# Optimization experiments

Hardware: AMD Instinct MI355X
Metric: run time of the kernel (lower is better)

## Reference

```python
import jax, jax.numpy as jnp
import numpy as np

B = 8192
NOISE = 25


def setup_inputs() -> dict:
    key = jax.random.key(0)
    ks = jax.random.split(key, 16)
    rn = lambda k, s: jax.random.normal(k, s, dtype=jnp.float32)
    return {
        "z": rn(ks[0], (B, 3)),
        "z_next": rn(ks[1], (B, 3)),
        "n": rn(ks[2], (B, NOISE)),
        "prior": rn(ks[3], (B, 4611)),
        "w1_W": rn(ks[4], (NOISE, 192)) * 0.2, "w1_b": rn(ks[5], (192,)) * 0.1,
        "b1_W": rn(ks[6], (NOISE, 64)) * 0.2, "b1_b": rn(ks[7], (64,)) * 0.1,
        "w2_W": rn(ks[8], (NOISE, 4096)) * 0.2, "w2_b": rn(ks[9], (4096,)) * 0.1,
        "b2_W": rn(ks[10], (NOISE, 64)) * 0.2, "b2_b": rn(ks[11], (64,)) * 0.1,
        "w3_W": rn(ks[12], (NOISE, 192)) * 0.2, "w3_b": rn(ks[13], (192,)) * 0.1,
        "b3_W": rn(ks[14], (NOISE, 3)) * 0.2, "b3_b": rn(ks[15], (3,)) * 0.1,
    }


def _pairwise_dist(A, Bm):
    # sqrt(sum_d (A_i - B_j)^2 + 1e-8) computed via the norm identity -> one GEMM
    sq = (jnp.sum(A * A, axis=1)[:, None]
          + jnp.sum(Bm * Bm, axis=1)[None, :]
          - 2.0 * (A @ Bm.T))
    return jnp.sqrt(jnp.maximum(sq, 0.0) + 1e-8)


def reference(z, z_next, n, prior,
              w1_W, w1_b, b1_W, b1_b,
              w2_W, w2_b, b2_W, b2_b,
              w3_W, w3_b, b3_W, b3_b):
    bs = z.shape[0]
    # hypernetwork: per-sample decoder weights from noise n (B, 25)
    W1 = (n @ w1_W + w1_b).reshape(bs, 64, 3)
    B1 = n @ b1_W + b1_b                       # (B, 64)
    W2 = (n @ w2_W + w2_b).reshape(bs, 64, 64)
    B2 = n @ b2_W + b2_b                       # (B, 64)
    W3 = (n @ w3_W + w3_b).reshape(bs, 3, 64)
    B3 = n @ b3_W + b3_b                       # (B, 3)
    # decode: per-sample bmm chain with ELU
    h = jax.nn.elu(jnp.einsum('bij,bj->bi', W1, z) + B1)
    h = jax.nn.elu(jnp.einsum('bij,bj->bi', W2, h) + B2)
    z_hat = jnp.einsum('bij,bj->bi', W3, h) + B3
    recon = jnp.mean(jnp.sum((z_hat - z_next) ** 2, axis=1))
    # KL estimator over flattened generated weights, D = 4611
    G = jnp.concatenate([W1.reshape(bs, -1), B1, W2.reshape(bs, -1), B2,
                         W3.reshape(bs, -1), B3], axis=1)
    wp = jnp.min(_pairwise_dist(prior, G), axis=0)   # nearest prior sample per gen sample
    idx = jnp.arange(bs)
    ww_mat = _pairwise_dist(G, G).at[idx, idx].add(1e10)
    ww = jnp.min(ww_mat, axis=0)
    D = G.shape[1]
    kl = jnp.mean(jnp.log(wp / (ww + 1e-8) + 1e-8)) * D
    kl = kl + jnp.log(jnp.float32(bs) / jnp.float32(bs - 1))
    return recon, kl, z_hat
```

## Files before the change

### kernel.cpp

```cpp
#include <hip/hip_runtime.h>
#include <math.h>

#define BATCH 8192
#define D_G   4611
#define DGP   4624
#define KN    25
#define KE    28

#define WS_WCAT   0
#define WS_BCAT   115600
#define WS_WCATT  120224
#define WS_M      249344
#define WS_C      249984
#define WS_BB     250016
#define WS_PPAD   250048
#define WS_Q      479424
#define WS_G2     487616
#define WS_RPAD   495808
#define WS_WP2    725184
#define WS_WW2    733376
#define WS_ACC    741568
#define WS_H1T    741600
#define WS_H2T    1265888

__device__ inline float eluf(float x) { return x > 0.f ? x : expm1f(x); }

__device__ __forceinline__ void gload_lds16(const float* g, float* l) {
  __builtin_amdgcn_global_load_lds((const __attribute__((address_space(1))) unsigned int*)g,
                                   (__attribute__((address_space(3))) unsigned int*)l, 16, 0, 0);
}

__device__ inline float sdot26(const float* __restrict__ WT, int rowidx, const float* nx) {
  const float* row = WT + (size_t)__builtin_amdgcn_readfirstlane(rowidx) * KE;
  float acc = row[25];
#pragma unroll
  for (int k = 0; k < 25; k++) acc = fmaf(row[k], nx[k], acc);
  return acc;
}

__global__ void k_init(float* ws) {
  int idx = blockIdx.x * 256 + threadIdx.x;
  unsigned int* u = (unsigned int*)ws;
  if (idx < BATCH)            u[WS_WP2 + idx] = 0x7F7FFFFFu;
  else if (idx < 2 * BATCH)   u[WS_WW2 + (idx - BATCH)] = 0x7F7FFFFFu;
  else if (idx == 2 * BATCH)  ws[WS_ACC] = 0.f;
}

__global__ void k_build(const float* __restrict__ w1W, const float* __restrict__ w1b,
                        const float* __restrict__ b1W, const float* __restrict__ b1b,
                        const float* __restrict__ w2W, const float* __restrict__ w2b,
                        const float* __restrict__ b2W, const float* __restrict__ b2b,
                        const float* __restrict__ w3W, const float* __restrict__ w3b,
                        const float* __restrict__ b3W, const float* __restrict__ b3b,
                        float* ws) {
  int idx = blockIdx.x * 256 + threadIdx.x;
  if (idx >= KN * D_G) return;
  int k = idx / D_G;
  int d = idx - k * D_G;
  float wv, bv;
  if (d < 192)       { int c = d;        wv = w1W[k*192  + c]; bv = w1b[c]; }
  else if (d < 256)  { int c = d - 192;  wv = b1W[k*64   + c]; bv = b1b[c]; }
  else if (d < 4352) { int c = d - 256;  wv = w2W[k*4096 + c]; bv = w2b[c]; }
  else if (d < 4416) { int c = d - 4352; wv = b2W[k*64   + c]; bv = b2b[c]; }
  else if (d < 4608) { int c = d - 4416; wv = w3W[k*192  + c]; bv = w3b[c]; }
  else               { int c = d - 4608; wv = b3W[k*3    + c]; bv = b3b[c]; }
  ws[WS_WCAT  + k * DGP + d] = wv;
  ws[WS_WCATT + d * KE  + k] = wv;
  if (k == 0) {
    ws[WS_BCAT + d] = bv;
    ws[WS_WCATT + d * KE + 25] = bv;
    ws[WS_WCATT + d * KE + 26] = 0.f;
    ws[WS_WCATT + d * KE + 27] = 0.f;
  }
}

__global__ __launch_bounds__(256) void k_M(float* ws) {
  const float* Wc = ws + WS_WCAT;
  const float* bc = ws + WS_BCAT;
  __shared__ float part[4][26];
  int a = blockIdx.x, t = threadIdx.x;
  int wv = t >> 6, l = t & 63;
  if (a < 25) {
    float acc[26];
#pragma unroll
    for (int v = 0; v < 26; v++) acc[v] = 0.f;
    for (int d = t; d < D_G; d += 256) {
      float va = Wc[a * DGP + d];
#pragma unroll
      for (int b = 0; b < 25; b++) acc[b] += va * Wc[b * DGP + d];
      acc[25] += va * bc[d];
    }
#pragma unroll
    for (int v = 0; v < 26; v++) {
      float x = acc[v];
#pragma unroll
      for (int off = 32; off > 0; off >>= 1) x += __shfl_down(x, off, 64);
      if (l == 0) part[wv][v] = x;
    }
    __syncthreads();
    if (t < 26) {
      float s = part[0][t] + part[1][t] + part[2][t] + part[3][t];
      if (t < 25) ws[WS_M + a * 25 + t] = s; else ws[WS_C + a] = s;
    }
  } else {
    float acc = 0.f;
    for (int d = t; d < D_G; d += 256) { float b = bc[d]; acc += b * b; }
#pragma unroll
    for (int off = 32; off > 0; off >>= 1) acc += __shfl_down(acc, off, 64);
    if (l == 0) part[wv][0] = acc;
    __syncthreads();
    if (t == 0) ws[WS_BB] = part[0][0] + part[1][0] + part[2][0] + part[3][0];
  }
}

__global__ void k_persample(const float* __restrict__ n, float* ws) {
  int j = blockIdx.x * 256 + threadIdx.x;
  if (j >= BATCH) return;
  const float* M  = ws + WS_M;
  const float* cv = ws + WS_C;
  float nr[25];
#pragma unroll
  for (int k = 0; k < 25; k++) nr[k] = n[j * 25 + k];
  float q = 0.f;
  for (int k2 = 0; k2 < 25; k2++) {
    float p = 0.f;
#pragma unroll
    for (int k1 = 0; k1 < 25; k1++) p += nr[k1] * M[k1 * 25 + k2];
    ws[WS_PPAD + j * KE + k2] = p;
    q += p * nr[k2];
  }
  float nc = 0.f;
#pragma unroll
  for (int k = 0; k < 25; k++) nc += nr[k] * cv[k];
  ws[WS_PPAD + j * KE + 25] = -0.5f * q;
  ws[WS_PPAD + j * KE + 26] = 0.f;
  ws[WS_PPAD + j * KE + 27] = 0.f;
  ws[WS_Q  + j] = q;
  ws[WS_G2 + j] = q + 2.f * nc + ws[WS_BB];
}

__global__ __launch_bounds__(256, 2) void k_prior(const float* __restrict__ prior, float* ws) {
  __shared__ float wlds[2][26 * 256 + 512];
  const float* wc = ws + WS_WCAT;
  const float* bc = ws + WS_BCAT;
  int t = threadIdx.x;
  int wv = t >> 6, l = t & 63;
  int i0 = (blockIdx.x * 4 + wv) * 4;
  const float* pr0 = prior + (size_t)i0 * D_G;

  float racc[4][25];
  float sacc[4], p2acc[4];
#pragma unroll
  for (int r = 0; r < 4; r++) {
    sacc[r] = 0.f; p2acc[r] = 0.f;
#pragma unroll
    for (int k = 0; k < 25; k++) racc[r][k] = 0.f;
  }

  float pvC[4][4], pvN[4][4];

#pragma unroll
  for (int u = 0; u < 7; u++) {
    int row = u * 4 + wv;
    if (row < 26)
      gload_lds16(wc + (size_t)row * DGP + 4 * l, &wlds[0][row * 256]);
  }
#pragma unroll
  for (int r = 0; r < 4; r++)
#pragma unroll
    for (int q = 0; q < 4; q++)
      pvN[r][q] = pr0[(size_t)r * D_G + 4 * l + q];

  for (int ch = 0; ch < 18; ++ch) {
    int cur = ch & 1;
    __syncthreads();
#pragma unroll
    for (int r = 0; r < 4; r++)
#pragma unroll
      for (int q = 0; q < 4; q++) pvC[r][q] = pvN[r][q];
    if (ch < 17) {
      int dnext = (ch + 1) * 256;
#pragma unroll
      for (int u = 0; u < 7; u++) {
        int row = u * 4 + wv;
        if (row < 26)
          gload_lds16(wc + (size_t)row * DGP + dnext + 4 * l, &wlds[cur ^ 1][row * 256]);
      }
#pragma unroll
      for (int r = 0; r < 4; r++)
#pragma unroll
        for (int q = 0; q < 4; q++)
          pvN[r][q] = pr0[(size_t)r * D_G + dnext + 4 * l + q];
    }
    const float* wb = wlds[cur];
    float4 bl = *(const float4*)&wb[25 * 256 + 4 * l];
#pragma unroll
    for (int r = 0; r < 4; r++) {
      p2acc[r] += pvC[r][0]*pvC[r][0] + pvC[r][1]*pvC[r][1] + pvC[r][2]*pvC[r][2] + pvC[r][3]*pvC[r][3];
      sacc[r]  += pvC[r][0]*bl.x + pvC[r][1]*bl.y + pvC[r][2]*bl.z + pvC[r][3]*bl.w;
    }
#pragma unroll
    for (int k = 0; k < 25; k++) {
      float4 w = *(const float4*)&wb[k * 256 + 4 * l];
#pragma unroll
      for (int r = 0; r < 4; r++)
        racc[r][k] += pvC[r][0]*w.x + pvC[r][1]*w.y + pvC[r][2]*w.z + pvC[r][3]*w.w;
    }
  }
  if (l < 3) {
    int d = 4608 + l;
#pragma unroll
    for (int r = 0; r < 4; r++) {
      float pvt = pr0[(size_t)r * D_G + d];
      p2acc[r] += pvt * pvt;
      sacc[r]  += pvt * bc[d];
#pragma unroll
      for (int k = 0; k < 25; k++) racc[r][k] += pvt * wc[(size_t)k * DGP + d];
    }
  }
#pragma unroll
  for (int r = 0; r < 4; r++) {
#pragma unroll
    for (int k = 0; k < 25; k++) {
      float v = racc[r][k];
#pragma unroll
      for (int off = 32; off > 0; off >>= 1) v += __shfl_down(v, off, 64);
      if (l == 0) ws[WS_RPAD + (size_t)(i0 + r) * KE + k] = v;
    }
    float s = sacc[r], p2 = p2acc[r];
#pragma unroll
    for (int off = 32; off > 0; off >>= 1) { s += __shfl_down(s, off, 64); p2 += __shfl_down(p2, off, 64); }
    if (l == 0) {
      ws[WS_RPAD + (size_t)(i0 + r) * KE + 25] = -0.5f * (p2 - 2.f * s);
      ws[WS_RPAD + (size_t)(i0 + r) * KE + 26] = 0.f;
      ws[WS_RPAD + (size_t)(i0 + r) * KE + 27] = 0.f;
    }
  }
}

template <int SKIP>
__global__ __launch_bounds__(256) void k_pair(const float* __restrict__ APAD,
                                              const float* __restrict__ Bn,
                                              const float* __restrict__ beta,
                                              unsigned int* __restrict__ outm) {
  __shared__ float rows[256 * KE] __attribute__((aligned(16)));
  int t = threadIdx.x;
  int jbase = blockIdx.y * 256;
  {
    const float4* src = (const float4*)(APAD + (size_t)jbase * KE);
    float4* dst = (float4*)rows;
#pragma unroll
    for (int u = 0; u < 7; u++) dst[t + 256 * u] = src[t + 256 * u];
  }
  int j0 = blockIdx.x * 512 + t;
  int j1 = j0 + 256;
  float nx0[25], nx1[25];
#pragma unroll
  for (int k = 0; k < 25; k++) { nx0[k] = Bn[j0 * 25 + k]; nx1[k] = Bn[j1 * 25 + k]; }
  float bj0 = beta[j0], bj1 = beta[j1];
  float mn0 = 3.402823466e38f, mn1 = 3.402823466e38f;
  __syncthreads();
#pragma unroll 2
  for (int it = 0; it < 256; ++it) {
    const float4* rv = (const float4*)(rows + it * KE);
    float rw[28];
#pragma unroll
    for (int u = 0; u < 7; u++) *(float4*)&rw[4 * u] = rv[u];
    float a0 = rw[25], a1 = rw[25];
#pragma unroll
    for (int k = 0; k < 25; k++) { a0 = fmaf(rw[k], nx0[k], a0); a1 = fmaf(rw[k], nx1[k], a1); }
    float sq0 = fmaxf(fmaf(-2.f, a0, bj0), 0.f);
    float sq1 = fmaxf(fmaf(-2.f, a1, bj1), 0.f);
    int i = jbase + it;
    bool sk0 = SKIP && (i == j0);
    bool sk1 = SKIP && (i == j1);
    mn0 = sk0 ? mn0 : fminf(mn0, sq0);
    mn1 = sk1 ? mn1 : fminf(mn1, sq1);
  }
  atomicMin(&outm[j0], __float_as_uint(mn0));
  atomicMin(&outm[j1], __float_as_uint(mn1));
}

__global__ __launch_bounds__(64) void kd1(const float* __restrict__ n, const float* __restrict__ z,
                                          const float* __restrict__ ws_wt, float* __restrict__ h1t) {
  int s = blockIdx.x * 64 + threadIdx.x;
  int rb = blockIdx.y * 16;
  float nx[25];
#pragma unroll
  for (int k = 0; k < 25; k++) nx[k] = n[s * 25 + k];
  float zr[3];
#pragma unroll
  for (int d = 0; d < 3; d++) zr[d] = z[s * 3 + d];
  for (int r = 0; r < 16; r++) {
    int rr = rb + r;
    float acc = sdot26(ws_wt, 192 + rr, nx);
#pragma unroll
    for (int d = 0; d < 3; d++)
      acc = fmaf(sdot26(ws_wt, rr * 3 + d, nx), zr[d], acc);
    h1t[rr * BATCH + s] = eluf(acc);
  }
}

__global__ __launch_bounds__(64) void kd2(const float* __restrict__ n,
                                          const float* __restrict__ ws_wt,
                                          const float* __restrict__ h1t, float* __restrict__ h2t) {
  int s = blockIdx.x * 64 + threadIdx.x;
  int rb = blockIdx.y * 4;
  float nx[25];
#pragma unroll
  for (int k = 0; k < 25; k++) nx[k] = n[s * 25 + k];
  float acc[4];
#pragma unroll
  for (int r = 0; r < 4; r++) acc[r] = sdot26(ws_wt, 4352 + rb + r, nx);
  for (int c = 0; c < 64; c++) {
    float h1c = h1t[c * BATCH + s];
#pragma unroll
    for (int r = 0; r < 4; r++) {
      float w = sdot26(ws_wt, 256 + (rb + r) * 64 + c, nx);
      acc[r] = fmaf(w, h1c, acc[r]);
    }
  }
#pragma unroll
  for (int r = 0; r < 4; r++) h2t[(rb + r) * BATCH + s] = eluf(acc[r]);
}

__global__ __launch_bounds__(64) void kd3(const float* __restrict__ n,
                                          const float* __restrict__ znext,
                                          const float* __restrict__ ws_wt,
                                          const float* __restrict__ h2t,
                                          float* __restrict__ out, float* __restrict__ accum) {
  int s = blockIdx.x * 64 + threadIdx.x;
  int r = blockIdx.y;
  float nx[25];
#pragma unroll
  for (int k = 0; k < 25; k++) nx[k] = n[s * 25 + k];
  float acc = sdot26(ws_wt, 4608 + r, nx);
  for (int c = 0; c < 64; c++)
    acc = fmaf(sdot26(ws_wt, 4416 + r * 64 + c, nx), h2t[c * BATCH + s], acc);
  out[2 + s * 3 + r] = acc;
  float dz = acc - znext[s * 3 + r];
  float v = dz * dz;
#pragma unroll
  for (int off = 32; off > 0; off >>= 1) v += __shfl_down(v, off, 64);
  if (threadIdx.x == 0) atomicAdd(accum, v);
}

__global__ void k_finish(float* ws, float* __restrict__ out) {
  __shared__ float sred[256];
  int t = threadIdx.x;
  float part = 0.f;
  for (int j = t; j < BATCH; j += 256) {
    float wp2 = ws[WS_WP2 + j];
    float ww2 = ws[WS_WW2 + j];
    float wp = sqrtf(wp2 + 1e-8f);
    float ww = sqrtf(ww2 + 1e-8f);
    part += logf(wp / (ww + 1e-8f) + 1e-8f);
  }
  sred[t] = part; __syncthreads();
  for (int off = 128; off > 0; off >>= 1) { if (t < off) sred[t] += sred[t + off]; __syncthreads(); }
  if (t == 0) {
    float kl = sred[0] / (float)BATCH * (float)D_G + logf((float)BATCH / (float)(BATCH - 1));
    out[0] = ws[WS_ACC] / (float)BATCH;
    out[1] = kl;
  }
}

extern "C" void kernel_launch(void* const* d_in, const int* in_sizes, int n_in,
                              void* d_out, int out_size, void* d_ws, size_t ws_size,
                              hipStream_t stream) {
  (void)in_sizes; (void)n_in; (void)out_size; (void)ws_size;
  const float* z     = (const float*)d_in[0];
  const float* znext = (const float*)d_in[1];
  const float* n     = (const float*)d_in[2];
  const float* prior = (const float*)d_in[3];
  const float* w1W = (const float*)d_in[4];  const float* w1b = (const float*)d_in[5];
  const float* b1W = (const float*)d_in[6];  const float* b1b = (const float*)d_in[7];
  const float* w2W = (const float*)d_in[8];  const float* w2b = (const float*)d_in[9];
  const float* b2W = (const float*)d_in[10]; const float* b2b = (const float*)d_in[11];
  const float* w3W = (const float*)d_in[12]; const float* w3b = (const float*)d_in[13];
  const float* b3W = (const float*)d_in[14]; const float* b3b = (const float*)d_in[15];
  float* out = (float*)d_out;
  float* ws  = (float*)d_ws;

  k_init<<<dim3(65), dim3(256), 0, stream>>>(ws);
  k_build<<<dim3((KN * D_G + 255) / 256), dim3(256), 0, stream>>>(
      w1W, w1b, b1W, b1b, w2W, w2b, b2W, b2b, w3W, w3b, b3W, b3b, ws);
  k_M<<<dim3(26), dim3(256), 0, stream>>>(ws);
  k_persample<<<dim3(32), dim3(256), 0, stream>>>(n, ws);
  k_prior<<<dim3(512), dim3(256), 0, stream>>>(prior, ws);
  k_pair<1><<<dim3(16, 32), dim3(256), 0, stream>>>(ws + WS_PPAD, n, ws + WS_Q,
                                                    (unsigned int*)(ws + WS_WW2));
  k_pair<0><<<dim3(16, 32), dim3(256), 0, stream>>>(ws + WS_RPAD, n, ws + WS_G2,
                                                    (unsigned int*)(ws + WS_WP2));
  kd1<<<dim3(128, 4), dim3(64), 0, stream>>>(n, z, ws + WS_WCATT, ws + WS_H1T);
  kd2<<<dim3(128, 16), dim3(64), 0, stream>>>(n, ws + WS_WCATT, ws + WS_H1T, ws + WS_H2T);
  kd3<<<dim3(128, 3), dim3(64), 0, stream>>>(n, znext, ws + WS_WCATT, ws + WS_H2T, out, ws + WS_ACC);
  k_finish<<<dim3(1), dim3(256), 0, stream>>>(ws, out);
}
```

Baseline: 546.4 us.

## Retile pairwise min kernel to 4 columns per thread with transposed noise

The pairwise-distance min kernel now gives each thread 4 columns instead of 2 and uses 128-row tiles instead of 256. This halves the LDS row tile and raises register reuse of each loaded row. Noise is stored transposed (k-major) in k_persample so the per-thread noise loads coalesce. The init kernel is folded into k_build to save a launch. The NT buffer aliases the H1T region, which is safe only because kd1 writes H1T after k_pair runs. Register pressure rises to about 100 noise values per thread, which could reduce occupancy.

```diff
diff --git a/kernel.cpp b/kernel.cpp
--- a/kernel.cpp
+++ b/kernel.cpp
@@ -21,6 +21,7 @@
 #define WS_WW2    733376
 #define WS_ACC    741568
 #define WS_H1T    741600
+#define WS_NT     741600
 #define WS_H2T    1265888
 
 __device__ inline float eluf(float x) { return x > 0.f ? x : expm1f(x); }
@@ -36,14 +37,6 @@
 #pragma unroll
   for (int k = 0; k < 25; k++) acc = fmaf(row[k], nx[k], acc);
   return acc;
-}
-
-__global__ void k_init(float* ws) {
-  int idx = blockIdx.x * 256 + threadIdx.x;
-  unsigned int* u = (unsigned int*)ws;
-  if (idx < BATCH)            u[WS_WP2 + idx] = 0x7F7FFFFFu;
-  else if (idx < 2 * BATCH)   u[WS_WW2 + (idx - BATCH)] = 0x7F7FFFFFu;
-  else if (idx == 2 * BATCH)  ws[WS_ACC] = 0.f;
 }
 
 __global__ void k_build(const float* __restrict__ w1W, const float* __restrict__ w1b,
@@ -54,6 +47,10 @@
                         const float* __restrict__ b3W, const float* __restrict__ b3b,
                         float* ws) {
   int idx = blockIdx.x * 256 + threadIdx.x;
+  unsigned int* u = (unsigned int*)ws;
+  if (idx < BATCH)            u[WS_WP2 + idx] = 0x7F7FFFFFu;
+  else if (idx < 2 * BATCH)   u[WS_WW2 + (idx - BATCH)] = 0x7F7FFFFFu;
+  else if (idx == 2 * BATCH)  ws[WS_ACC] = 0.f;
   if (idx >= KN * D_G) return;
   int k = idx / D_G;
   int d = idx - k * D_G;
@@ -121,6 +118,8 @@
   float nr[25];
 #pragma unroll
   for (int k = 0; k < 25; k++) nr[k] = n[j * 25 + k];
+#pragma unroll
+  for (int k = 0; k < 25; k++) ws[WS_NT + k * BATCH + j] = nr[k];
   float q = 0.f;
   for (int k2 = 0; k2 < 25; k2++) {
     float p = 0.f;
@@ -240,45 +239,60 @@
 
 template <int SKIP>
 __global__ __launch_bounds__(256) void k_pair(const float* __restrict__ APAD,
-                                              const float* __restrict__ Bn,
+                                              const float* __restrict__ nT,
                                               const float* __restrict__ beta,
                                               unsigned int* __restrict__ outm) {
-  __shared__ float rows[256 * KE] __attribute__((aligned(16)));
+  __shared__ float rows[128 * KE] __attribute__((aligned(16)));
   int t = threadIdx.x;
-  int jbase = blockIdx.y * 256;
+  int ibase = blockIdx.y * 128;
   {
-    const float4* src = (const float4*)(APAD + (size_t)jbase * KE);
+    const float4* src = (const float4*)(APAD + (size_t)ibase * KE);
     float4* dst = (float4*)rows;
 #pragma unroll
-    for (int u = 0; u < 7; u++) dst[t + 256 * u] = src[t + 256 * u];
-  }
-  int j0 = blockIdx.x * 512 + t;
-  int j1 = j0 + 256;
-  float nx0[25], nx1[25];
-#pragma unroll
-  for (int k = 0; k < 25; k++) { nx0[k] = Bn[j0 * 25 + k]; nx1[k] = Bn[j1 * 25 + k]; }
-  float bj0 = beta[j0], bj1 = beta[j1];
-  float mn0 = 3.402823466e38f, mn1 = 3.402823466e38f;
+    for (int u = 0; u < 4; u++) {
+      int idx = t + 256 * u;
+      if (idx < 896) dst[idx] = src[idx];
+    }
+  }
+  int j0 = blockIdx.x * 1024 + t;
+  float nx0[25], nx1[25], nx2[25], nx3[25];
+#pragma unroll
+  for (int k = 0; k < 25; k++) {
+    nx0[k] = nT[k * BATCH + j0];
+    nx1[k] = nT[k * BATCH + j0 + 256];
+    nx2[k] = nT[k * BATCH + j0 + 512];
+    nx3[k] = nT[k * BATCH + j0 + 768];
+  }
+  float bj0 = beta[j0], bj1 = beta[j0 + 256], bj2 = beta[j0 + 512], bj3 = beta[j0 + 768];
+  float mn0 = 3.402823466e38f, mn1 = mn0, mn2 = mn0, mn3 = mn0;
   __syncthreads();
-#pragma unroll 2
-  for (int it = 0; it < 256; ++it) {
+  for (int it = 0; it < 128; ++it) {
     const float4* rv = (const float4*)(rows + it * KE);
     float rw[28];
 #pragma unroll
     for (int u = 0; u < 7; u++) *(float4*)&rw[4 * u] = rv[u];
-    float a0 = rw[25], a1 = rw[25];
-#pragma unroll
-    for (int k = 0; k < 25; k++) { a0 = fmaf(rw[k], nx0[k], a0); a1 = fmaf(rw[k], nx1[k], a1); }
+    float a0 = rw[25], a1 = rw[25], a2 = rw[25], a3 = rw[25];
+#pragma unroll
+    for (int k = 0; k < 25; k++) {
+      a0 = fmaf(rw[k], nx0[k], a0);
+      a1 = fmaf(rw[k], nx1[k], a1);
+      a2 = fmaf(rw[k], nx2[k], a2);
+      a3 = fmaf(rw[k], nx3[k], a3);
+    }
     float sq0 = fmaxf(fmaf(-2.f, a0, bj0), 0.f);
     float sq1 = fmaxf(fmaf(-2.f, a1, bj1), 0.f);
-    int i = jbase + it;
-    bool sk0 = SKIP && (i == j0);
-    bool sk1 = SKIP && (i == j1);
-    mn0 = sk0 ? mn0 : fminf(mn0, sq0);
-    mn1 = sk1 ? mn1 : fminf(mn1, sq1);
-  }
-  atomicMin(&outm[j0], __float_as_uint(mn0));
-  atomicMin(&outm[j1], __float_as_uint(mn1));
+    float sq2 = fmaxf(fmaf(-2.f, a2, bj2), 0.f);
+    float sq3 = fmaxf(fmaf(-2.f, a3, bj3), 0.f);
+    int i = ibase + it;
+    mn0 = (SKIP && i == j0)       ? mn0 : fminf(mn0, sq0);
+    mn1 = (SKIP && i == j0 + 256) ? mn1 : fminf(mn1, sq1);
+    mn2 = (SKIP && i == j0 + 512) ? mn2 : fminf(mn2, sq2);
+    mn3 = (SKIP && i == j0 + 768) ? mn3 : fminf(mn3, sq3);
+  }
+  atomicMin(&outm[j0],       __float_as_uint(mn0));
+  atomicMin(&outm[j0 + 256], __float_as_uint(mn1));
+  atomicMin(&outm[j0 + 512], __float_as_uint(mn2));
+  atomicMin(&outm[j0 + 768], __float_as_uint(mn3));
 }
 
 __global__ __launch_bounds__(64) void kd1(const float* __restrict__ n, const float* __restrict__ z,
@@ -382,16 +396,15 @@
   float* out = (float*)d_out;
   float* ws  = (float*)d_ws;
 
-  k_init<<<dim3(65), dim3(256), 0, stream>>>(ws);
   k_build<<<dim3((KN * D_G + 255) / 256), dim3(256), 0, stream>>>(
       w1W, w1b, b1W, b1b, w2W, w2b, b2W, b2b, w3W, w3b, b3W, b3b, ws);
   k_M<<<dim3(26), dim3(256), 0, stream>>>(ws);
   k_persample<<<dim3(32), dim3(256), 0, stream>>>(n, ws);
   k_prior<<<dim3(512), dim3(256), 0, stream>>>(prior, ws);
-  k_pair<1><<<dim3(16, 32), dim3(256), 0, stream>>>(ws + WS_PPAD, n, ws + WS_Q,
-                                                    (unsigned int*)(ws + WS_WW2));
-  k_pair<0><<<dim3(16, 32), dim3(256), 0, stream>>>(ws + WS_RPAD, n, ws + WS_G2,
-                                                    (unsigned int*)(ws + WS_WP2));
+  k_pair<1><<<dim3(8, 64), dim3(256), 0, stream>>>(ws + WS_PPAD, ws + WS_NT, ws + WS_Q,
+                                                   (unsigned int*)(ws + WS_WW2));
+  k_pair<0><<<dim3(8, 64), dim3(256), 0, stream>>>(ws + WS_RPAD, ws + WS_NT, ws + WS_G2,
+                                                   (unsigned int*)(ws + WS_WP2));
   kd1<<<dim3(128, 4), dim3(64), 0, stream>>>(n, z, ws + WS_WCATT, ws + WS_H1T);
   kd2<<<dim3(128, 16), dim3(64), 0, stream>>>(n, ws + WS_WCATT, ws + WS_H1T, ws + WS_H2T);
   kd3<<<dim3(128, 3), dim3(64), 0, stream>>>(n, znext, ws + WS_WCATT, ws + WS_H2T, out, ws + WS_ACC);
```

Measured after the change: 562.0 us. 1.03x slower.
